# Performance work log

Measured on AMD Instinct MI355X. Metric: run time of the kernel, lower is better.

The kernel has to match this reference:

```python
import jax, jax.numpy as jnp
import numpy as np


def setup_inputs() -> dict:
    key = jax.random.key(0)
    ks = jax.random.split(key, 6)
    B, S, D_IN, D_OUT, E, R = 4, 2048, 4096, 4096, 8, 16
    x = jax.random.normal(ks[0], (B, S, D_IN), dtype=jnp.float32)
    probs = jax.random.uniform(ks[1], (B, E), dtype=jnp.float32)
    router_probs = probs / jnp.sum(probs, axis=-1, keepdims=True)
    weight = jax.random.normal(ks[2], (D_OUT, D_IN), dtype=jnp.float32) * 0.02
    bias = jax.random.normal(ks[3], (D_OUT,), dtype=jnp.float32) * 0.02
    lora_A = jax.random.normal(ks[4], (E, R, D_IN), dtype=jnp.float32) * 0.02
    lora_B = jax.random.normal(ks[5], (E, D_OUT, R), dtype=jnp.float32) * 0.02
    return {"x": x, "router_probs": router_probs, "weight": weight,
            "bias": bias, "lora_A": lora_A, "lora_B": lora_B}


def reference(x, router_probs, weight, bias, lora_A, lora_B):
    scaling = 2.0
    # base linear: [b,s,i] @ [o,i]^T + bias
    base_out = jnp.einsum('bsi,oi->bso', x, weight) + bias
    # low-rank per-expert projection: [b,s,e,r] (small: r=16)
    mid = jnp.einsum('bsi,eri->bser', x, lora_A)
    # weight by router probs (per batch, per expert) before up-projection
    mid_w = mid * router_probs[:, None, :, None]
    # sum over experts fused into the up-projection contraction
    delta = jnp.einsum('bser,eor->bso', mid_w, lora_B) * scaling
    return base_out + delta
```

## Files before the change

### kernel.cpp

```cpp
#include <hip/hip_runtime.h>


typedef _Float16 half8 __attribute__((ext_vector_type(8)));
typedef _Float16 half4 __attribute__((ext_vector_type(4)));
typedef float    f32x4 __attribute__((ext_vector_type(4)));

#define M_TOT 8192
#define N_TOT 4096
#define K_IN  4096
#define KA    4224
#define NT    66

__device__ __forceinline__ void cvt_store4(_Float16* p, float4 f) {
  half4 h;
  h[0] = (_Float16)f.x; h[1] = (_Float16)f.y;
  h[2] = (_Float16)f.z; h[3] = (_Float16)f.w;
  *(half4*)p = h;
}

template <int LOG2C, int DCOLS>
__global__ __launch_bounds__(256) void convert_f32_f16_t(
    const float* __restrict__ src, _Float16* __restrict__ dst, int total8) {
  for (int i = blockIdx.x * 256 + threadIdx.x; i < total8;
       i += gridDim.x * 256) {
    int base = i << 3;
    int r = base >> LOG2C;
    int c = base & ((1 << LOG2C) - 1);
    const float4* s = (const float4*)(src + (size_t)base);
    float4 f0 = s[0], f1 = s[1];
    half8 h;
    h[0]=(_Float16)f0.x; h[1]=(_Float16)f0.y; h[2]=(_Float16)f0.z; h[3]=(_Float16)f0.w;
    h[4]=(_Float16)f1.x; h[5]=(_Float16)f1.y; h[6]=(_Float16)f1.z; h[7]=(_Float16)f1.w;
    *(half8*)(dst + (size_t)r * DCOLS + c) = h;
  }
}

__global__ __launch_bounds__(256) void wtail_gather_f16(
    const float* __restrict__ loraB, _Float16* __restrict__ Wa) {
  int idx = blockIdx.x * 256 + threadIdx.x;
  int n = idx >> 7, j = idx & 127;
  int e = j >> 4, r = j & 15;
  Wa[(size_t)n * KA + K_IN + j] =
      (_Float16)loraB[((size_t)e * N_TOT + n) * 16 + r];
}

__global__ __launch_bounds__(256) void lorabf_gather_f32(
    const float* __restrict__ loraB, float* __restrict__ lorabf) {
  int idx = blockIdx.x * 256 + threadIdx.x;
  int n = idx >> 7, j = idx & 127;
  int e = j >> 4, r = j & 15;
  lorabf[(size_t)n * 128 + j] = loraB[((size_t)e * N_TOT + n) * 16 + r];
}

__global__ __launch_bounds__(256) void mid2_kernel(
    _Float16* __restrict__ Xa, const _Float16* __restrict__ lAh,
    const float* __restrict__ router) {
  __shared__ _Float16 As[32 * 64];
  __shared__ _Float16 Bs[128 * 64];
  int tid = threadIdx.x, lane = tid & 63, w = tid >> 6;
  int m0 = blockIdx.x * 32;
  int b = m0 >> 11;
  f32x4 acc[2][2] = {};

  for (int ks = 0; ks < 64; ++ks) {
    int kb = ks * 128;
    {
      const char* s = (const char*)Xa +
          (size_t)(m0 + w * 8 + (lane >> 3)) * (KA * 2) + kb + (lane & 7) * 16;
      __builtin_amdgcn_global_load_lds(
          (const __attribute__((address_space(1))) void*)s,
          (__attribute__((address_space(3))) void*)((char*)As + w * 1024), 16, 0, 0);
    }
#pragma unroll
    for (int i = 0; i < 4; ++i) {
      const char* s = (const char*)lAh +
          (size_t)((w * 4 + i) * 8 + (lane >> 3)) * (4096 * 2) + kb + (lane & 7) * 16;
      __builtin_amdgcn_global_load_lds(
          (const __attribute__((address_space(1))) void*)s,
          (__attribute__((address_space(3))) void*)((char*)Bs + (w * 4 + i) * 1024), 16, 0, 0);
    }
    __syncthreads();
#pragma unroll
    for (int kk = 0; kk < 2; ++kk) {
      half8 a[2], bf[2];
#pragma unroll
      for (int mi = 0; mi < 2; ++mi)
        a[mi] = *(const half8*)(As + (mi * 16 + (lane & 15)) * 64 + kk * 32 + (lane >> 4) * 8);
#pragma unroll
      for (int ni = 0; ni < 2; ++ni)
        bf[ni] = *(const half8*)(Bs + (w * 32 + ni * 16 + (lane & 15)) * 64 + kk * 32 + (lane >> 4) * 8);
#pragma unroll
      for (int mi = 0; mi < 2; ++mi)
#pragma unroll
        for (int ni = 0; ni < 2; ++ni)
          acc[mi][ni] = __builtin_amdgcn_mfma_f32_16x16x32_f16(a[mi], bf[ni], acc[mi][ni], 0, 0, 0);
    }
    __syncthreads();
  }

#pragma unroll
  for (int ni = 0; ni < 2; ++ni) {
    int j = w * 32 + ni * 16 + (lane & 15);
    int e = j >> 4;
    float sc = 2.0f * router[b * 8 + e];
#pragma unroll
    for (int mi = 0; mi < 2; ++mi) {
      f32x4 v = acc[mi][ni];
#pragma unroll
      for (int jj = 0; jj < 4; ++jj) {
        int m = m0 + mi * 16 + (lane >> 4) * 4 + jj;
        Xa[(size_t)m * KA + K_IN + j] = (_Float16)(v[jj] * sc);
      }
    }
  }
}

__global__ __launch_bounds__(256) void mid_kernel(
    const float* __restrict__ x, const float* __restrict__ loraA,
    const float* __restrict__ router, float* __restrict__ midw) {
  __shared__ _Float16 As[32 * 64];
  __shared__ _Float16 Bs[128 * 64];
  int tid = threadIdx.x, lane = tid & 63, w = tid >> 6;
  int m0 = blockIdx.x * 32;
  int b = m0 >> 11;
  f32x4 acc[2][2] = {};
  for (int ks = 0; ks < 64; ++ks) {
    int k0 = ks * 64;
#pragma unroll
    for (int it = 0; it < 2; ++it) {
      int idx = tid + it * 256;
      int r = idx >> 4, c4 = idx & 15;
      float4 f = *(const float4*)(x + (size_t)(m0 + r) * K_IN + k0 + c4 * 4);
      cvt_store4(As + r * 64 + c4 * 4, f);
    }
#pragma unroll
    for (int it = 0; it < 8; ++it) {
      int idx = tid + it * 256;
      int r = idx >> 4, c4 = idx & 15;
      float4 f = *(const float4*)(loraA + (size_t)r * K_IN + k0 + c4 * 4);
      cvt_store4(Bs + r * 64 + c4 * 4, f);
    }
    __syncthreads();
#pragma unroll
    for (int kk = 0; kk < 2; ++kk) {
      half8 a[2], bf[2];
#pragma unroll
      for (int mi = 0; mi < 2; ++mi)
        a[mi] = *(const half8*)(As + (mi * 16 + (lane & 15)) * 64 + kk * 32 + (lane >> 4) * 8);
#pragma unroll
      for (int ni = 0; ni < 2; ++ni)
        bf[ni] = *(const half8*)(Bs + (w * 32 + ni * 16 + (lane & 15)) * 64 + kk * 32 + (lane >> 4) * 8);
#pragma unroll
      for (int mi = 0; mi < 2; ++mi)
#pragma unroll
        for (int ni = 0; ni < 2; ++ni)
          acc[mi][ni] = __builtin_amdgcn_mfma_f32_16x16x32_f16(a[mi], bf[ni], acc[mi][ni], 0, 0, 0);
    }
    __syncthreads();
  }
#pragma unroll
  for (int ni = 0; ni < 2; ++ni) {
    int j = w * 32 + ni * 16 + (lane & 15);
    int e = j >> 4;
    float sc = 2.0f * router[b * 8 + e];
#pragma unroll
    for (int mi = 0; mi < 2; ++mi) {
      f32x4 v = acc[mi][ni];
#pragma unroll
      for (int jj = 0; jj < 4; ++jj) {
        int m = m0 + mi * 16 + (lane >> 4) * 4 + jj;
        midw[(size_t)m * 128 + j] = v[jj] * sc;
      }
    }
  }
}

#define BAR    __builtin_amdgcn_s_barrier()
#define SCHED0 __builtin_amdgcn_sched_barrier(0)
#define PRIO1  __builtin_amdgcn_s_setprio(1)
#define PRIO0  __builtin_amdgcn_s_setprio(0)
#define LGKM0  do { asm volatile("s_waitcnt lgkmcnt(0)" ::: "memory"); \
                    __builtin_amdgcn_sched_barrier(0); } while (0)
#define VMW4   asm volatile("s_waitcnt vmcnt(4)" ::: "memory")
#define VMW0   asm volatile("s_waitcnt vmcnt(0)" ::: "memory")
#define GLOAD(src, dst) __builtin_amdgcn_global_load_lds( \
    (const __attribute__((address_space(1))) void*)(src), \
    (__attribute__((address_space(3))) void*)(dst), 16, 0, 0)

#define STAGEH(srcbase, t1, kh, plane) do { \
  const char* s_ = (srcbase) + (size_t)(t1) * 128 + (kh) * 64; \
  GLOAD(s_ + goff0, (char*)(plane) + loff0); \
  GLOAD(s_ + goff1, (char*)(plane) + loff1); \
  } while (0)

#define READ_A4(aF, mb, plane) do { \
  _Pragma("unroll") for (int mi = 0; mi < 4; ++mi) \
    aF[mi] = *(const half8*)((const char*)(plane) + \
                             (wm + ((mb) + mi) * 16 + ln15) * 64 + rslot); \
  } while (0)

#define READ_B4(bF, plane) do { \
  _Pragma("unroll") for (int ni = 0; ni < 4; ++ni) \
    bF[ni] = *(const half8*)((const char*)(plane) + \
                             (wn + ni * 16 + ln15) * 64 + rslot); \
  } while (0)

#define MFMA_Q16(aF, bF, mb) do { \
  PRIO1; \
  _Pragma("unroll") for (int mi = 0; mi < 4; ++mi) \
    _Pragma("unroll") for (int ni = 0; ni < 4; ++ni) \
      acc[(mb) + mi][ni] = __builtin_amdgcn_mfma_f32_16x16x32_f16( \
          aF[mi], bF[ni], acc[(mb) + mi][ni], 0, 0, 0); \
  PRIO0; \
  } while (0)

__global__ __launch_bounds__(512, 2) void gemm256(
    const _Float16* __restrict__ Xa, const _Float16* __restrict__ Wa,
    const float* __restrict__ bias, float* __restrict__ out) {
  __shared__ _Float16 As[2][2][256 * 32];
  __shared__ _Float16 Bs[2][2][256 * 32];

  int tid = threadIdx.x, lane = tid & 63, w = tid >> 6;
  int ln15 = lane & 15, ln4 = lane >> 4;
  int wm = (w >> 2) * 128, wn = (w & 3) * 64;

  int bid = blockIdx.x;
  int xcd = bid & 7, idx = bid >> 3;
  int mt = (xcd & 3) * 8 + (idx & 7);
  int nt = (xcd >> 2) * 8 + (idx >> 3);
  int m0 = mt << 8, n0 = nt << 8;

  const char* XpC = (const char*)Xa + (size_t)m0 * (KA * 2);
  const char* WpC = (const char*)Wa + (size_t)n0 * (KA * 2);

  int sslot16 = (((lane & 3) ^ ((lane >> 3) & 3)) * 16);
  int goff0 = ((2 * w + 0) * 16 + (lane >> 2)) * (KA * 2) + sslot16;
  int goff1 = ((2 * w + 1) * 16 + (lane >> 2)) * (KA * 2) + sslot16;
  int loff0 = (2 * w + 0) * 1024 + lane * 16;
  int loff1 = (2 * w + 1) * 1024 + lane * 16;

  int rslot = ((ln4 ^ ((lane >> 1) & 3)) * 16);

  f32x4 acc[8][4] = {};
  half8 aF[4], bF[4];

  STAGEH(XpC, 0, 0, As[0][0]); STAGEH(WpC, 0, 0, Bs[0][0]);
  STAGEH(XpC, 0, 1, As[0][1]); STAGEH(WpC, 0, 1, Bs[0][1]);
  VMW0; BAR; SCHED0;

#pragma unroll 1
  for (int t = 0; t < NT; ++t) {
    int cur = t & 1, nxt = cur ^ 1;
    bool pf = (t < NT - 1);

    READ_A4(aF, 0, As[cur][0]);
    READ_B4(bF, Bs[cur][0]);
    if (pf) STAGEH(XpC, t + 1, 0, As[nxt][0]);
    BAR; LGKM0; MFMA_Q16(aF, bF, 0); BAR;

    READ_A4(aF, 4, As[cur][0]);
    if (pf) STAGEH(WpC, t + 1, 0, Bs[nxt][0]);
    BAR; LGKM0; MFMA_Q16(aF, bF, 4);
    if (pf) { VMW4; } else { VMW0; }
    BAR; SCHED0;

    READ_A4(aF, 0, As[cur][1]);
    READ_B4(bF, Bs[cur][1]);
    if (pf) STAGEH(XpC, t + 1, 1, As[nxt][1]);
    BAR; LGKM0; MFMA_Q16(aF, bF, 0); BAR;

    READ_A4(aF, 4, As[cur][1]);
    if (pf) STAGEH(WpC, t + 1, 1, Bs[nxt][1]);
    BAR; LGKM0; MFMA_Q16(aF, bF, 4);
    if (pf) { VMW4; BAR; SCHED0; }
  }

#pragma unroll
  for (int ni = 0; ni < 4; ++ni) {
    int n = n0 + wn + ni * 16 + ln15;
    float bz = bias[n];
#pragma unroll
    for (int mi = 0; mi < 8; ++mi) {
      f32x4 v = acc[mi][ni];
      int mb = m0 + wm + mi * 16 + ln4 * 4;
#pragma unroll
      for (int jj = 0; jj < 4; ++jj)
        out[(size_t)(mb + jj) * N_TOT + n] = v[jj] + bz;
    }
  }
}

__global__ __launch_bounds__(256) void gemm_fallback(
    const float* __restrict__ x, const float* __restrict__ wgt,
    const float* __restrict__ midw, const float* __restrict__ lorabf,
    const float* __restrict__ bias, float* __restrict__ out) {
  __shared__ _Float16 As[128 * 64];
  __shared__ _Float16 Bs[128 * 64];
  int tid = threadIdx.x, lane = tid & 63, w = tid >> 6;
  int mt = blockIdx.x & 63, nt = blockIdx.x >> 6;
  int m0 = mt << 7, n0 = nt << 7;
  int wm = (w >> 1) * 64, wn = (w & 1) * 64;
  f32x4 acc[4][4] = {};
  for (int ks = 0; ks < NT; ++ks) {
    int k0 = ks * 64;
    const float *asrc, *bsrc; size_t astr, bstr; int ac, bc;
    if (ks < 64) { asrc = x;    astr = K_IN; ac = k0;        bsrc = wgt;    bstr = K_IN; bc = k0; }
    else         { asrc = midw; astr = 128;  ac = k0 - K_IN; bsrc = lorabf; bstr = 128;  bc = k0 - K_IN; }
#pragma unroll
    for (int it = 0; it < 8; ++it) {
      int idx = tid + it * 256;
      int r = idx >> 4, c4 = idx & 15;
      float4 fa = *(const float4*)(asrc + (size_t)(m0 + r) * astr + ac + c4 * 4);
      cvt_store4(As + r * 64 + c4 * 4, fa);
      float4 fb = *(const float4*)(bsrc + (size_t)(n0 + r) * bstr + bc + c4 * 4);
      cvt_store4(Bs + r * 64 + c4 * 4, fb);
    }
    __syncthreads();
#pragma unroll
    for (int kk = 0; kk < 2; ++kk) {
      half8 a[4], bf[4];
#pragma unroll
      for (int mi = 0; mi < 4; ++mi)
        a[mi] = *(const half8*)(As + (wm + mi * 16 + (lane & 15)) * 64 + kk * 32 + (lane >> 4) * 8);
#pragma unroll
      for (int ni = 0; ni < 4; ++ni)
        bf[ni] = *(const half8*)(Bs + (wn + ni * 16 + (lane & 15)) * 64 + kk * 32 + (lane >> 4) * 8);
#pragma unroll
      for (int mi = 0; mi < 4; ++mi)
#pragma unroll
        for (int ni = 0; ni < 4; ++ni)
          acc[mi][ni] = __builtin_amdgcn_mfma_f32_16x16x32_f16(a[mi], bf[ni], acc[mi][ni], 0, 0, 0);
    }
    __syncthreads();
  }
#pragma unroll
  for (int ni = 0; ni < 4; ++ni) {
    int n = n0 + wn + ni * 16 + (lane & 15);
    float bz = bias[n];
#pragma unroll
    for (int mi = 0; mi < 4; ++mi) {
      f32x4 v = acc[mi][ni];
      int mbase = m0 + wm + mi * 16 + (lane >> 4) * 4;
#pragma unroll
      for (int jj = 0; jj < 4; ++jj)
        out[(size_t)(mbase + jj) * N_TOT + n] = v[jj] + bz;
    }
  }
}

extern "C" void kernel_launch(void* const* d_in, const int* in_sizes, int n_in,
                              void* d_out, int out_size, void* d_ws, size_t ws_size,
                              hipStream_t stream) {
  const float* x      = (const float*)d_in[0];
  const float* router = (const float*)d_in[1];
  const float* wgt    = (const float*)d_in[2];
  const float* bias   = (const float*)d_in[3];
  const float* loraA  = (const float*)d_in[4];
  const float* loraB  = (const float*)d_in[5];
  float* out = (float*)d_out;
  char* ws = (char*)d_ws;

  const size_t XAUG_B = (size_t)M_TOT * KA * 2;
  const size_t WAUG_B = (size_t)N_TOT * KA * 2;
  const size_t LAH_B  = (size_t)128 * K_IN * 2;
  const size_t MIDW_B = (size_t)M_TOT * 128 * 4;
  bool fast = ws_size >= XAUG_B + WAUG_B + LAH_B;

  if (fast) {
    _Float16* Xa  = (_Float16*)ws;
    _Float16* Wa  = (_Float16*)(ws + XAUG_B);
    _Float16* lAh = (_Float16*)(ws + XAUG_B + WAUG_B);
    convert_f32_f16_t<12, KA><<<2048, 256, 0, stream>>>(x,   Xa, M_TOT * K_IN / 8);
    convert_f32_f16_t<12, KA><<<2048, 256, 0, stream>>>(wgt, Wa, N_TOT * K_IN / 8);
    convert_f32_f16_t<12, 4096><<<256, 256, 0, stream>>>(loraA, lAh, 128 * K_IN / 8);
    wtail_gather_f16<<<2048, 256, 0, stream>>>(loraB, Wa);
    mid2_kernel<<<256, 256, 0, stream>>>(Xa, lAh, router);
    gemm256<<<512, 512, 0, stream>>>(Xa, Wa, bias, out);
  } else {
    float* midw   = (float*)ws;
    float* lorabf = (float*)(ws + MIDW_B);
    lorabf_gather_f32<<<2048, 256, 0, stream>>>(loraB, lorabf);
    mid_kernel<<<256, 256, 0, stream>>>(x, loraA, router, midw);
    gemm_fallback<<<2048, 256, 0, stream>>>(x, wgt, midw, lorabf, bias, out);
  }
}
```

Baseline: 406.0 us.

## Replace double-buffered GEMM loop with a 4-stage LDS ring pipeline

The main fp16 GEMM moves from a two-buffer scheme over half K-tiles, with several barriers per step, to a 4-slot ring of 32-wide K slices. Three slices are kept in flight, and each slice has one barrier and a single 8x4 MFMA block. The aim is to hide global-load latency better and cut barrier and LDS-wait overhead per MFMA. In exchange, LDS use grows to 128 KB per block and more A fragments stay live in registers. That likely leaves room for only one resident block per CU instead of two, despite the launch bound of 2.

Measured after the change: 377.0 us. -7.1%, faster.

```diff
diff --git a/kernel.cpp b/kernel.cpp
--- a/kernel.cpp
+++ b/kernel.cpp
@@ -9,7 +9,7 @@
 #define N_TOT 4096
 #define K_IN  4096
 #define KA    4224
-#define NT    66
+#define NT    132
 
 __device__ __forceinline__ void cvt_store4(_Float16* p, float4 f) {
   half4 h;
@@ -181,44 +181,50 @@
 #define PRIO0  __builtin_amdgcn_s_setprio(0)
 #define LGKM0  do { asm volatile("s_waitcnt lgkmcnt(0)" ::: "memory"); \
                     __builtin_amdgcn_sched_barrier(0); } while (0)
+#define VMW8   asm volatile("s_waitcnt vmcnt(8)" ::: "memory")
 #define VMW4   asm volatile("s_waitcnt vmcnt(4)" ::: "memory")
 #define VMW0   asm volatile("s_waitcnt vmcnt(0)" ::: "memory")
 #define GLOAD(src, dst) __builtin_amdgcn_global_load_lds( \
     (const __attribute__((address_space(1))) void*)(src), \
     (__attribute__((address_space(3))) void*)(dst), 16, 0, 0)
 
-#define STAGEH(srcbase, t1, kh, plane) do { \
-  const char* s_ = (srcbase) + (size_t)(t1) * 128 + (kh) * 64; \
-  GLOAD(s_ + goff0, (char*)(plane) + loff0); \
-  GLOAD(s_ + goff1, (char*)(plane) + loff1); \
-  } while (0)
-
-#define READ_A4(aF, mb, plane) do { \
-  _Pragma("unroll") for (int mi = 0; mi < 4; ++mi) \
-    aF[mi] = *(const half8*)((const char*)(plane) + \
-                             (wm + ((mb) + mi) * 16 + ln15) * 64 + rslot); \
-  } while (0)
-
-#define READ_B4(bF, plane) do { \
+#define READS(SL) do { \
+  _Pragma("unroll") for (int mi = 0; mi < 8; ++mi) \
+    aF[mi] = *(const half8*)(LDS + (SL) * 16384 + \
+                             (wm + mi * 16 + ln15) * 64 + rslot); \
   _Pragma("unroll") for (int ni = 0; ni < 4; ++ni) \
-    bF[ni] = *(const half8*)((const char*)(plane) + \
+    bF[ni] = *(const half8*)(LDS + 65536 + (SL) * 16384 + \
                              (wn + ni * 16 + ln15) * 64 + rslot); \
   } while (0)
 
-#define MFMA_Q16(aF, bF, mb) do { \
+#define STAGE4(TT, SL) do { \
+  const char* sA_ = XpC + (size_t)(TT) * 64; \
+  const char* sB_ = WpC + (size_t)(TT) * 64; \
+  GLOAD(sA_ + goff0, LDS + (SL) * 16384 + l0); \
+  GLOAD(sA_ + goff1, LDS + (SL) * 16384 + l1); \
+  GLOAD(sB_ + goff0, LDS + 65536 + (SL) * 16384 + l0); \
+  GLOAD(sB_ + goff1, LDS + 65536 + (SL) * 16384 + l1); \
+  } while (0)
+
+#define MFMA32 do { \
   PRIO1; \
-  _Pragma("unroll") for (int mi = 0; mi < 4; ++mi) \
+  _Pragma("unroll") for (int mi = 0; mi < 8; ++mi) \
     _Pragma("unroll") for (int ni = 0; ni < 4; ++ni) \
-      acc[(mb) + mi][ni] = __builtin_amdgcn_mfma_f32_16x16x32_f16( \
-          aF[mi], bF[ni], acc[(mb) + mi][ni], 0, 0, 0); \
+      acc[mi][ni] = __builtin_amdgcn_mfma_f32_16x16x32_f16( \
+          aF[mi], bF[ni], acc[mi][ni], 0, 0, 0); \
   PRIO0; \
+  } while (0)
+
+#define TILE_FULL(SL) do { \
+  READS(SL); \
+  STAGE4(t4 + (SL) + 3, ((SL) + 3) & 3); \
+  LGKM0; MFMA32; VMW8; BAR; SCHED0; \
   } while (0)
 
 __global__ __launch_bounds__(512, 2) void gemm256(
     const _Float16* __restrict__ Xa, const _Float16* __restrict__ Wa,
     const float* __restrict__ bias, float* __restrict__ out) {
-  __shared__ _Float16 As[2][2][256 * 32];
-  __shared__ _Float16 Bs[2][2][256 * 32];
+  __shared__ __align__(16) char LDS[131072];
 
   int tid = threadIdx.x, lane = tid & 63, w = tid >> 6;
   int ln15 = lane & 15, ln4 = lane >> 4;
@@ -233,47 +239,28 @@
   const char* XpC = (const char*)Xa + (size_t)m0 * (KA * 2);
   const char* WpC = (const char*)Wa + (size_t)n0 * (KA * 2);
 
-  int sslot16 = (((lane & 3) ^ ((lane >> 3) & 3)) * 16);
-  int goff0 = ((2 * w + 0) * 16 + (lane >> 2)) * (KA * 2) + sslot16;
-  int goff1 = ((2 * w + 1) * 16 + (lane >> 2)) * (KA * 2) + sslot16;
-  int loff0 = (2 * w + 0) * 1024 + lane * 16;
-  int loff1 = (2 * w + 1) * 1024 + lane * 16;
+  int i0 = tid, i1 = tid + 512;
+  int goff0 = (i0 >> 2) * (KA * 2) + (((i0 & 3) ^ ((i0 >> 3) & 3)) * 16);
+  int goff1 = (i1 >> 2) * (KA * 2) + (((i1 & 3) ^ ((i1 >> 3) & 3)) * 16);
+  int l0 = i0 * 16, l1 = i1 * 16;
 
   int rslot = ((ln4 ^ ((lane >> 1) & 3)) * 16);
 
   f32x4 acc[8][4] = {};
-  half8 aF[4], bF[4];
-
-  STAGEH(XpC, 0, 0, As[0][0]); STAGEH(WpC, 0, 0, Bs[0][0]);
-  STAGEH(XpC, 0, 1, As[0][1]); STAGEH(WpC, 0, 1, Bs[0][1]);
-  VMW0; BAR; SCHED0;
+  half8 aF[8], bF[4];
+
+  STAGE4(0, 0); STAGE4(1, 1); STAGE4(2, 2);
+  VMW8; BAR; SCHED0;
 
 #pragma unroll 1
-  for (int t = 0; t < NT; ++t) {
-    int cur = t & 1, nxt = cur ^ 1;
-    bool pf = (t < NT - 1);
-
-    READ_A4(aF, 0, As[cur][0]);
-    READ_B4(bF, Bs[cur][0]);
-    if (pf) STAGEH(XpC, t + 1, 0, As[nxt][0]);
-    BAR; LGKM0; MFMA_Q16(aF, bF, 0); BAR;
-
-    READ_A4(aF, 4, As[cur][0]);
-    if (pf) STAGEH(WpC, t + 1, 0, Bs[nxt][0]);
-    BAR; LGKM0; MFMA_Q16(aF, bF, 4);
-    if (pf) { VMW4; } else { VMW0; }
-    BAR; SCHED0;
-
-    READ_A4(aF, 0, As[cur][1]);
-    READ_B4(bF, Bs[cur][1]);
-    if (pf) STAGEH(XpC, t + 1, 1, As[nxt][1]);
-    BAR; LGKM0; MFMA_Q16(aF, bF, 0); BAR;
-
-    READ_A4(aF, 4, As[cur][1]);
-    if (pf) STAGEH(WpC, t + 1, 1, Bs[nxt][1]);
-    BAR; LGKM0; MFMA_Q16(aF, bF, 4);
-    if (pf) { VMW4; BAR; SCHED0; }
-  }
+  for (int t4 = 0; t4 < NT - 4; t4 += 4) {
+    TILE_FULL(0); TILE_FULL(1); TILE_FULL(2); TILE_FULL(3);
+  }
+
+  { READS(0); STAGE4(131, 3); LGKM0; MFMA32; VMW8; BAR; SCHED0; }
+  { READS(1); LGKM0; MFMA32; VMW4; BAR; SCHED0; }
+  { READS(2); LGKM0; MFMA32; VMW0; BAR; SCHED0; }
+  { READS(3); LGKM0; MFMA32; }
 
 #pragma unroll
   for (int ni = 0; ni < 4; ++ni) {
@@ -301,7 +288,7 @@
   int m0 = mt << 7, n0 = nt << 7;
   int wm = (w >> 1) * 64, wn = (w & 1) * 64;
   f32x4 acc[4][4] = {};
-  for (int ks = 0; ks < NT; ++ks) {
+  for (int ks = 0; ks < 66; ++ks) {
     int k0 = ks * 64;
     const float *asrc, *bsrc; size_t astr, bstr; int ac, bc;
     if (ks < 64) { asrc = x;    astr = K_IN; ac = k0;        bsrc = wgt;    bstr = K_IN; bc = k0; }
```
